# Optimization experiments

Hardware: AMD Instinct MI355X
Metric: run time of the kernel (lower is better)

Reference implementation:

```python
import jax, jax.numpy as jnp
import numpy as np

B, N, DIN, DOUT = 32, 1024, 256, 256


def setup_inputs() -> dict:
    key = jax.random.key(0)
    ks = jax.random.split(key, 7)
    s = 1.0 / np.sqrt(DIN)
    return {
        "x": jax.random.normal(ks[0], (B, N, DIN), dtype=jnp.float32),
        "Wq": jax.random.uniform(ks[1], (DOUT, DIN), minval=-s, maxval=s, dtype=jnp.float32),
        "bq": jax.random.uniform(ks[2], (DOUT,), minval=-s, maxval=s, dtype=jnp.float32),
        "Wk": jax.random.uniform(ks[3], (DOUT, DIN), minval=-s, maxval=s, dtype=jnp.float32),
        "bk": jax.random.uniform(ks[4], (DOUT,), minval=-s, maxval=s, dtype=jnp.float32),
        "Wv": jax.random.uniform(ks[5], (DOUT, DIN), minval=-s, maxval=s, dtype=jnp.float32),
        "bv": jax.random.uniform(ks[6], (DOUT,), minval=-s, maxval=s, dtype=jnp.float32),
    }


def reference(x, Wq, bq, Wk, bk, Wv, bv):
    # q, k, v: (B, N, Dout)
    q = jnp.einsum("bnd,od->bno", x, Wq) + bq
    k = jnp.einsum("bnd,od->bno", x, Wk) + bk
    v = jnp.einsum("bnd,od->bno", x, Wv) + bv
    # logits: (B, N, N) = q @ k^T per batch
    logits = jnp.einsum("bnd,bmd->bnm", q, k)
    # NOTE: softmax over the BATCH dim (axis=0), as in the original module
    attn = jax.nn.softmax(logits, axis=0)
    out = jnp.einsum("bnm,bmd->bnd", attn, v)  # (B, N, Dout)
    return out
```

## Files before the change

### kernel.cpp

```cpp
#include <hip/hip_runtime.h>

typedef __bf16 bf16x8 __attribute__((ext_vector_type(8)));
typedef __bf16 bf16x4 __attribute__((ext_vector_type(4)));
typedef float  f32x4  __attribute__((ext_vector_type(4)));

#define BM 128
#define BN 128
#define BK 64
#define LSD 144

__device__ __forceinline__ void g2l16(const void* g, void* l) {
    __builtin_amdgcn_global_load_lds((const __attribute__((address_space(1))) void*)g,
                                     (__attribute__((address_space(3))) void*)l, 16, 0, 0);
}

template<int EPI, int SWZ>
__global__ __launch_bounds__(256)
void gemm_nt(const __bf16* __restrict__ A, const __bf16* __restrict__ B,
             void* __restrict__ Cv, const float* __restrict__ bias,
             int lda, int ldb, int ldc, int K,
             long sA, long sB, long sC)
{
    __shared__ __align__(16) __bf16 smem[128 * LSD];
    __bf16* As = smem;
    __bf16* Bs = smem + BM * BK;

    const int tid  = threadIdx.x;
    const int w    = tid >> 6;
    const int lane = tid & 63;
    const int quad = lane >> 4;
    const int l16  = lane & 15;
    const int wm   = w & 1;
    const int wn   = w >> 1;

    int m0, n0, z;
    if constexpr (SWZ == 1) {
        const int id = blockIdx.x;
        const int x  = id & 7, s = id >> 3;
        z = x + ((s >> 6) << 3);
        const int t = s & 63;
        m0 = (t & 7) * BM;
        n0 = (t >> 3) * BN;
    } else {
        m0 = blockIdx.x * BM;
        n0 = blockIdx.y * BN;
        z  = blockIdx.z;
    }

    const __bf16* Ab = A + (size_t)z * sA;
    const __bf16* Bb = B + (size_t)z * sB;

    const int srow = (w << 3) + (lane >> 3);
    const int scol = ((lane & 7) ^ (lane >> 3)) << 3;
    char* ldsA = (char*)As + (size_t)w * 1024;
    char* ldsB = (char*)Bs + (size_t)w * 1024;

    const __bf16* Ag = Ab + (size_t)(m0 + srow) * lda + scol;
    const __bf16* Bg = Bb + (size_t)(n0 + srow) * ldb + scol;

    f32x4 acc[4][4] = {};

    for (int k0 = 0; k0 < K; k0 += BK) {
        __syncthreads();
        #pragma unroll
        for (int c = 0; c < 4; c++)
            g2l16(Ag + (size_t)(c * 32) * lda + k0, ldsA + c * 4096);
        #pragma unroll
        for (int c = 0; c < 4; c++)
            g2l16(Bg + (size_t)(c * 32) * ldb + k0, ldsB + c * 4096);
        __syncthreads();

        #pragma unroll
        for (int kk = 0; kk < BK; kk += 32) {
            const int ub = kk >> 3;
            bf16x8 a[4], b[4];
            #pragma unroll
            for (int mt = 0; mt < 4; mt++) {
                const int row = wm * 64 + mt * 16 + l16;
                const int cp  = ((quad + ub) ^ (row & 7)) << 3;
                a[mt] = *(const bf16x8*)&As[row * BK + cp];
            }
            #pragma unroll
            for (int nt = 0; nt < 4; nt++) {
                const int row = wn * 64 + nt * 16 + l16;
                const int cp  = ((quad + ub) ^ (row & 7)) << 3;
                b[nt] = *(const bf16x8*)&Bs[row * BK + cp];
            }
            #pragma unroll
            for (int mt = 0; mt < 4; mt++)
                #pragma unroll
                for (int nt = 0; nt < 4; nt++)
                    acc[mt][nt] = __builtin_amdgcn_mfma_f32_16x16x32_bf16(
                        a[mt], b[nt], acc[mt][nt], 0, 0, 0);
        }
    }

    __syncthreads();

    if constexpr (EPI == 2) {
        #pragma unroll
        for (int mt = 0; mt < 4; mt++) {
            const int rl = wm * 64 + mt * 16 + quad * 4;
            #pragma unroll
            for (int nt = 0; nt < 4; nt++) {
                const int cl = wn * 64 + nt * 16 + l16;
                #pragma unroll
                for (int r = 0; r < 4; r++)
                    smem[(rl + r) * LSD + cl] = (__bf16)__expf(acc[mt][nt][r]);
            }
        }
        __syncthreads();
        __bf16* C = (__bf16*)Cv + (size_t)z * sC;
        #pragma unroll
        for (int i = 0; i < 8; i++) {
            const int c   = tid + i * 256;
            const int row = c >> 4, c8 = (c & 15) << 3;
            *(bf16x8*)&C[(size_t)(m0 + row) * ldc + n0 + c8] =
                *(const bf16x8*)&smem[row * LSD + c8];
        }
    } else {
        if (z < 2) {
            #pragma unroll
            for (int mt = 0; mt < 4; mt++) {
                const int rl = wm * 64 + mt * 16 + quad * 4;
                #pragma unroll
                for (int nt = 0; nt < 4; nt++) {
                    const int cl = wn * 64 + nt * 16 + l16;
                    const float bn = bias[z * 256 + n0 + cl];
                    #pragma unroll
                    for (int r = 0; r < 4; r++)
                        smem[(rl + r) * LSD + cl] = (__bf16)(acc[mt][nt][r] + bn);
                }
            }
            __syncthreads();
            __bf16* C = (__bf16*)Cv + (size_t)z * sC;
            #pragma unroll
            for (int i = 0; i < 8; i++) {
                const int c   = tid + i * 256;
                const int row = c >> 4, c8 = (c & 15) << 3;
                *(bf16x8*)&C[(size_t)(m0 + row) * ldc + n0 + c8] =
                    *(const bf16x8*)&smem[row * LSD + c8];
            }
        } else {
            #pragma unroll
            for (int mt = 0; mt < 4; mt++) {
                const int ml = wm * 64 + mt * 16 + quad * 4;
                #pragma unroll
                for (int nt = 0; nt < 4; nt++) {
                    const int dl = wn * 64 + nt * 16 + l16;
                    const float bn = bias[z * 256 + n0 + dl];
                    bf16x4 pk;
                    #pragma unroll
                    for (int r = 0; r < 4; r++) pk[r] = (__bf16)(acc[mt][nt][r] + bn);
                    *(bf16x4*)&smem[dl * LSD + ml] = pk;
                }
            }
            __syncthreads();
            __bf16* C = (__bf16*)Cv + 2 * sC;
            const int bidx = m0 >> 10, mbase = m0 & 1023;
            #pragma unroll
            for (int i = 0; i < 8; i++) {
                const int c  = tid + i * 256;
                const int dl = c >> 4, m8 = (c & 15) << 3;
                *(bf16x8*)&C[(size_t)bidx * 262144 + (size_t)(n0 + dl) * 1024 + mbase + m8] =
                    *(const bf16x8*)&smem[dl * LSD + m8];
            }
        }
    }
}

__global__ __launch_bounds__(256)
void gemm_pv(const __bf16* __restrict__ E, const __bf16* __restrict__ vT,
             float* __restrict__ out)
{
    __shared__ __align__(16) __bf16 As[128 * 64];
    __shared__ __align__(16) __bf16 Bs[64 * 64];

    const int tid  = threadIdx.x;
    const int w    = tid >> 6;
    const int lane = tid & 63;
    const int quad = lane >> 4;
    const int l16  = lane & 15;
    const int wm   = w & 1;
    const int wn   = w >> 1;

    const int id = blockIdx.x;
    const int x  = id & 7, s = id >> 3;
    const int z  = x + ((s >> 5) << 3);
    const int t  = s & 31;
    const int m0 = (t & 7) * 128;
    const int n0 = (t >> 3) * 64;

    const __bf16* Eb = E  + (size_t)z * 1048576;
    const __bf16* Vb = vT + (size_t)z * 262144;
    float*        Ob = out + (size_t)z * 262144;

    const int srow = (w << 3) + (lane >> 3);
    const int scol = ((lane & 7) ^ (lane >> 3)) << 3;
    char* ldsA = (char*)As + (size_t)w * 1024;
    char* ldsB = (char*)Bs + (size_t)w * 1024;

    const __bf16* Ag = Eb + (size_t)(m0 + srow) * 1024 + scol;
    const __bf16* Bg = Vb + (size_t)(n0 + srow) * 1024 + scol;

    f32x4 acc[4][2] = {};

    for (int k0 = 0; k0 < 1024; k0 += BK) {
        __syncthreads();
        #pragma unroll
        for (int c = 0; c < 4; c++)
            g2l16(Ag + (size_t)(c * 32) * 1024 + k0, ldsA + c * 4096);
        #pragma unroll
        for (int c = 0; c < 2; c++)
            g2l16(Bg + (size_t)(c * 32) * 1024 + k0, ldsB + c * 4096);
        __syncthreads();

        #pragma unroll
        for (int kk = 0; kk < BK; kk += 32) {
            const int ub = kk >> 3;
            bf16x8 a[4], b[2];
            #pragma unroll
            for (int mt = 0; mt < 4; mt++) {
                const int row = wm * 64 + mt * 16 + l16;
                const int cp  = ((quad + ub) ^ (row & 7)) << 3;
                a[mt] = *(const bf16x8*)&As[row * BK + cp];
            }
            #pragma unroll
            for (int nt = 0; nt < 2; nt++) {
                const int row = wn * 32 + nt * 16 + l16;
                const int cp  = ((quad + ub) ^ (row & 7)) << 3;
                b[nt] = *(const bf16x8*)&Bs[row * BK + cp];
            }
            #pragma unroll
            for (int mt = 0; mt < 4; mt++)
                #pragma unroll
                for (int nt = 0; nt < 2; nt++)
                    acc[mt][nt] = __builtin_amdgcn_mfma_f32_16x16x32_bf16(
                        a[mt], b[nt], acc[mt][nt], 0, 0, 0);
        }
    }

    #pragma unroll
    for (int mt = 0; mt < 4; mt++) {
        const int mb = m0 + wm * 64 + mt * 16 + quad * 4;
        #pragma unroll
        for (int nt = 0; nt < 2; nt++) {
            const int n = n0 + wn * 32 + nt * 16 + l16;
            #pragma unroll
            for (int r = 0; r < 4; r++)
                Ob[(size_t)(mb + r) * 256 + n] = acc[mt][nt][r];
        }
    }
}

__global__ __launch_bounds__(256)
void cvt_all(const float* __restrict__ x,
             const float* __restrict__ Wq, const float* __restrict__ Wk,
             const float* __restrict__ Wv,
             const float* __restrict__ bq, const float* __restrict__ bk,
             const float* __restrict__ bv,
             __bf16* __restrict__ xb, __bf16* __restrict__ Wqb,
             float* __restrict__ bpack)
{
    const int i = blockIdx.x * 256 + threadIdx.x;
    if (i < 1073152) {
        const float* s; __bf16* d; int off;
        if (i < 1048576)      { s = x;  d = xb;            off = i; }
        else if (i < 1056768) { s = Wq; d = Wqb;           off = i - 1048576; }
        else if (i < 1064960) { s = Wk; d = Wqb + 131072;  off = i - 1056768; }
        else                  { s = Wv; d = Wqb + 262144;  off = i - 1064960; }
        const float4* s4 = (const float4*)s;
        const float4 f0 = s4[off * 2], f1 = s4[off * 2 + 1];
        bf16x8 o;
        o[0] = (__bf16)f0.x; o[1] = (__bf16)f0.y; o[2] = (__bf16)f0.z; o[3] = (__bf16)f0.w;
        o[4] = (__bf16)f1.x; o[5] = (__bf16)f1.y; o[6] = (__bf16)f1.z; o[7] = (__bf16)f1.w;
        ((bf16x8*)d)[off] = o;
    } else if (i < 1073344) {
        const int j = i - 1073152;
        const int sel = j >> 6, jj = j & 63;
        const float* s = sel == 0 ? bq : (sel == 1 ? bk : bv);
        ((float4*)bpack)[j] = ((const float4*)s)[jj];
    }
}

__global__ __launch_bounds__(256)
void softmax_norm(__bf16* __restrict__ E)
{
    const size_t p = (size_t)blockIdx.x * 256 + threadIdx.x;
    bf16x8* E8 = (bf16x8*)E;
    bf16x8 e[32];
    #pragma unroll
    for (int b = 0; b < 32; b++) e[b] = E8[(size_t)b * 131072 + p];
    float s[8] = {0.f, 0.f, 0.f, 0.f, 0.f, 0.f, 0.f, 0.f};
    #pragma unroll
    for (int b = 0; b < 32; b++)
        #pragma unroll
        for (int j = 0; j < 8; j++) s[j] += (float)e[b][j];
    float rs[8];
    #pragma unroll
    for (int j = 0; j < 8; j++) rs[j] = __builtin_amdgcn_rcpf(s[j]);
    #pragma unroll
    for (int b = 0; b < 32; b++) {
        bf16x8 o = e[b];
        #pragma unroll
        for (int j = 0; j < 8; j++) o[j] = (__bf16)((float)o[j] * rs[j]);
        E8[(size_t)b * 131072 + p] = o;
    }
}

extern "C" void kernel_launch(void* const* d_in, const int* in_sizes, int n_in,
                              void* d_out, int out_size, void* d_ws, size_t ws_size,
                              hipStream_t stream)
{
    const float* x  = (const float*)d_in[0];
    const float* Wq = (const float*)d_in[1];
    const float* bq = (const float*)d_in[2];
    const float* Wk = (const float*)d_in[3];
    const float* bk = (const float*)d_in[4];
    const float* Wv = (const float*)d_in[5];
    const float* bv = (const float*)d_in[6];
    float* out = (float*)d_out;

    char* ws = (char*)d_ws;
    __bf16* xb    = (__bf16*)(ws);
    __bf16* qkv   = (__bf16*)(ws + (16u << 20));
    __bf16* E     = (__bf16*)(ws + (64u << 20));
    __bf16* Wqb   = (__bf16*)(ws + (128u << 20));
    float*  bpack = (float*) (ws + (128u << 20) + (3u << 18));

    cvt_all<<<4194, 256, 0, stream>>>(x, Wq, Wk, Wv, bq, bk, bv, xb, Wqb, bpack);

    gemm_nt<4, 0><<<dim3(256, 2, 3), 256, 0, stream>>>(xb, Wqb, qkv, bpack,
                                                       256, 256, 256, 256,
                                                       0, 131072, 8388608);

    gemm_nt<2, 1><<<2048, 256, 0, stream>>>(qkv, qkv + 8388608, E, nullptr,
                                            256, 256, 1024, 256,
                                            262144, 262144, 1048576);

    softmax_norm<<<512, 256, 0, stream>>>(E);

    gemm_pv<<<1024, 256, 0, stream>>>(E, qkv + 2 * 8388608, out);
}
```

Measured before the change: 197.8 us.

## Fuse fp32-to-bf16 conversion into projection and softmax normalization into PV GEMM

Removes the separate conversion kernel by loading fp32 x and weights directly in the projection GEMM and converting to bf16 before the LDS store. The softmax pass now only computes per-position reciprocal sums into a bf16 buffer, and the PV GEMM scales E by those reciprocals while staging tiles, so E is never rewritten. PV tiles grow to 128x128, halving the grid. The trade is that the fused loads become register-staged instead of direct global-to-LDS, and PV now reads an extra 1024x1024 reciprocal matrix per tile.

```diff
diff --git a/kernel.cpp b/kernel.cpp
--- a/kernel.cpp
+++ b/kernel.cpp
@@ -4,9 +4,7 @@
 typedef __bf16 bf16x4 __attribute__((ext_vector_type(4)));
 typedef float  f32x4  __attribute__((ext_vector_type(4)));
 
-#define BM 128
-#define BN 128
-#define BK 64
+#define BK  64
 #define LSD 144
 
 __device__ __forceinline__ void g2l16(const void* g, void* l) {
@@ -14,16 +12,18 @@
                                      (__attribute__((address_space(3))) void*)l, 16, 0, 0);
 }
 
-template<int EPI, int SWZ>
+
 __global__ __launch_bounds__(256)
-void gemm_nt(const __bf16* __restrict__ A, const __bf16* __restrict__ B,
-             void* __restrict__ Cv, const float* __restrict__ bias,
-             int lda, int ldb, int ldc, int K,
-             long sA, long sB, long sC)
+void gemm_proj(const float* __restrict__ x,
+               const float* __restrict__ Wq, const float* __restrict__ Wk,
+               const float* __restrict__ Wv,
+               const float* __restrict__ bq, const float* __restrict__ bk,
+               const float* __restrict__ bv,
+               __bf16* __restrict__ qkv)
 {
     __shared__ __align__(16) __bf16 smem[128 * LSD];
     __bf16* As = smem;
-    __bf16* Bs = smem + BM * BK;
+    __bf16* Bs = smem + 128 * BK;
 
     const int tid  = threadIdx.x;
     const int w    = tid >> 6;
@@ -33,41 +33,43 @@
     const int wm   = w & 1;
     const int wn   = w >> 1;
 
-    int m0, n0, z;
-    if constexpr (SWZ == 1) {
-        const int id = blockIdx.x;
-        const int x  = id & 7, s = id >> 3;
-        z = x + ((s >> 6) << 3);
-        const int t = s & 63;
-        m0 = (t & 7) * BM;
-        n0 = (t >> 3) * BN;
-    } else {
-        m0 = blockIdx.x * BM;
-        n0 = blockIdx.y * BN;
-        z  = blockIdx.z;
-    }
-
-    const __bf16* Ab = A + (size_t)z * sA;
-    const __bf16* Bb = B + (size_t)z * sB;
+    const int m0 = blockIdx.x * 128;
+    const int n0 = blockIdx.y * 128;
+    const int z  = blockIdx.z;
+
+    const float* W    = z == 0 ? Wq : (z == 1 ? Wk : Wv);
+    const float* bias = z == 0 ? bq : (z == 1 ? bk : bv);
 
     const int srow = (w << 3) + (lane >> 3);
     const int scol = ((lane & 7) ^ (lane >> 3)) << 3;
-    char* ldsA = (char*)As + (size_t)w * 1024;
-    char* ldsB = (char*)Bs + (size_t)w * 1024;
-
-    const __bf16* Ag = Ab + (size_t)(m0 + srow) * lda + scol;
-    const __bf16* Bg = Bb + (size_t)(n0 + srow) * ldb + scol;
+    char* ldsA = (char*)As + w * 1024 + lane * 16;
+    char* ldsB = (char*)Bs + w * 1024 + lane * 16;
+
+    const float* Ag = x + (size_t)(m0 + srow) * 256 + scol;
+    const float* Bg = W + (size_t)(n0 + srow) * 256 + scol;
 
     f32x4 acc[4][4] = {};
 
-    for (int k0 = 0; k0 < K; k0 += BK) {
-        __syncthreads();
-        #pragma unroll
-        for (int c = 0; c < 4; c++)
-            g2l16(Ag + (size_t)(c * 32) * lda + k0, ldsA + c * 4096);
-        #pragma unroll
-        for (int c = 0; c < 4; c++)
-            g2l16(Bg + (size_t)(c * 32) * ldb + k0, ldsB + c * 4096);
+    for (int k0 = 0; k0 < 256; k0 += BK) {
+        __syncthreads();
+        #pragma unroll
+        for (int c = 0; c < 4; c++) {
+            const float* s = Ag + (size_t)(c * 32) * 256 + k0;
+            const float4 f0 = *(const float4*)s, f1 = *(const float4*)(s + 4);
+            bf16x8 o;
+            o[0] = (__bf16)f0.x; o[1] = (__bf16)f0.y; o[2] = (__bf16)f0.z; o[3] = (__bf16)f0.w;
+            o[4] = (__bf16)f1.x; o[5] = (__bf16)f1.y; o[6] = (__bf16)f1.z; o[7] = (__bf16)f1.w;
+            *(bf16x8*)(ldsA + c * 4096) = o;
+        }
+        #pragma unroll
+        for (int c = 0; c < 4; c++) {
+            const float* s = Bg + (size_t)(c * 32) * 256 + k0;
+            const float4 f0 = *(const float4*)s, f1 = *(const float4*)(s + 4);
+            bf16x8 o;
+            o[0] = (__bf16)f0.x; o[1] = (__bf16)f0.y; o[2] = (__bf16)f0.z; o[3] = (__bf16)f0.w;
+            o[4] = (__bf16)f1.x; o[5] = (__bf16)f1.y; o[6] = (__bf16)f1.z; o[7] = (__bf16)f1.w;
+            *(bf16x8*)(ldsB + c * 4096) = o;
+        }
         __syncthreads();
 
         #pragma unroll
@@ -96,85 +98,62 @@
     }
 
     __syncthreads();
-
-    if constexpr (EPI == 2) {
+    if (z < 2) {
         #pragma unroll
         for (int mt = 0; mt < 4; mt++) {
             const int rl = wm * 64 + mt * 16 + quad * 4;
             #pragma unroll
             for (int nt = 0; nt < 4; nt++) {
                 const int cl = wn * 64 + nt * 16 + l16;
+                const float bn = bias[n0 + cl];
                 #pragma unroll
                 for (int r = 0; r < 4; r++)
-                    smem[(rl + r) * LSD + cl] = (__bf16)__expf(acc[mt][nt][r]);
-            }
-        }
-        __syncthreads();
-        __bf16* C = (__bf16*)Cv + (size_t)z * sC;
+                    smem[(rl + r) * LSD + cl] = (__bf16)(acc[mt][nt][r] + bn);
+            }
+        }
+        __syncthreads();
+        __bf16* C = qkv + (size_t)z * 8388608;
         #pragma unroll
         for (int i = 0; i < 8; i++) {
             const int c   = tid + i * 256;
             const int row = c >> 4, c8 = (c & 15) << 3;
-            *(bf16x8*)&C[(size_t)(m0 + row) * ldc + n0 + c8] =
+            *(bf16x8*)&C[(size_t)(m0 + row) * 256 + n0 + c8] =
                 *(const bf16x8*)&smem[row * LSD + c8];
         }
     } else {
-        if (z < 2) {
-            #pragma unroll
-            for (int mt = 0; mt < 4; mt++) {
-                const int rl = wm * 64 + mt * 16 + quad * 4;
-                #pragma unroll
-                for (int nt = 0; nt < 4; nt++) {
-                    const int cl = wn * 64 + nt * 16 + l16;
-                    const float bn = bias[z * 256 + n0 + cl];
-                    #pragma unroll
-                    for (int r = 0; r < 4; r++)
-                        smem[(rl + r) * LSD + cl] = (__bf16)(acc[mt][nt][r] + bn);
-                }
-            }
-            __syncthreads();
-            __bf16* C = (__bf16*)Cv + (size_t)z * sC;
-            #pragma unroll
-            for (int i = 0; i < 8; i++) {
-                const int c   = tid + i * 256;
-                const int row = c >> 4, c8 = (c & 15) << 3;
-                *(bf16x8*)&C[(size_t)(m0 + row) * ldc + n0 + c8] =
-                    *(const bf16x8*)&smem[row * LSD + c8];
-            }
-        } else {
-            #pragma unroll
-            for (int mt = 0; mt < 4; mt++) {
-                const int ml = wm * 64 + mt * 16 + quad * 4;
-                #pragma unroll
-                for (int nt = 0; nt < 4; nt++) {
-                    const int dl = wn * 64 + nt * 16 + l16;
-                    const float bn = bias[z * 256 + n0 + dl];
-                    bf16x4 pk;
-                    #pragma unroll
-                    for (int r = 0; r < 4; r++) pk[r] = (__bf16)(acc[mt][nt][r] + bn);
-                    *(bf16x4*)&smem[dl * LSD + ml] = pk;
-                }
-            }
-            __syncthreads();
-            __bf16* C = (__bf16*)Cv + 2 * sC;
-            const int bidx = m0 >> 10, mbase = m0 & 1023;
-            #pragma unroll
-            for (int i = 0; i < 8; i++) {
-                const int c  = tid + i * 256;
-                const int dl = c >> 4, m8 = (c & 15) << 3;
-                *(bf16x8*)&C[(size_t)bidx * 262144 + (size_t)(n0 + dl) * 1024 + mbase + m8] =
-                    *(const bf16x8*)&smem[dl * LSD + m8];
-            }
+        #pragma unroll
+        for (int mt = 0; mt < 4; mt++) {
+            const int ml = wm * 64 + mt * 16 + quad * 4;
+            #pragma unroll
+            for (int nt = 0; nt < 4; nt++) {
+                const int dl = wn * 64 + nt * 16 + l16;
+                const float bn = bias[n0 + dl];
+                bf16x4 pk;
+                #pragma unroll
+                for (int r = 0; r < 4; r++) pk[r] = (__bf16)(acc[mt][nt][r] + bn);
+                *(bf16x4*)&smem[dl * LSD + ml] = pk;
+            }
+        }
+        __syncthreads();
+        __bf16* C = qkv + 2 * 8388608;
+        const int bidx = m0 >> 10, mbase = m0 & 1023;
+        #pragma unroll
+        for (int i = 0; i < 8; i++) {
+            const int c  = tid + i * 256;
+            const int dl = c >> 4, m8 = (c & 15) << 3;
+            *(bf16x8*)&C[(size_t)bidx * 262144 + (size_t)(n0 + dl) * 1024 + mbase + m8] =
+                *(const bf16x8*)&smem[dl * LSD + m8];
         }
     }
 }
 
 __global__ __launch_bounds__(256)
-void gemm_pv(const __bf16* __restrict__ E, const __bf16* __restrict__ vT,
-             float* __restrict__ out)
-{
-    __shared__ __align__(16) __bf16 As[128 * 64];
-    __shared__ __align__(16) __bf16 Bs[64 * 64];
+void gemm_logits(const __bf16* __restrict__ Q, const __bf16* __restrict__ Km,
+                 __bf16* __restrict__ E)
+{
+    __shared__ __align__(16) __bf16 smem[128 * LSD];
+    __bf16* As = smem;
+    __bf16* Bs = smem + 128 * BK;
 
     const int tid  = threadIdx.x;
     const int w    = tid >> 6;
@@ -186,39 +165,38 @@
 
     const int id = blockIdx.x;
     const int x  = id & 7, s = id >> 3;
-    const int z  = x + ((s >> 5) << 3);
-    const int t  = s & 31;
+    const int z  = x + ((s >> 6) << 3);
+    const int t  = s & 63;
     const int m0 = (t & 7) * 128;
-    const int n0 = (t >> 3) * 64;
-
-    const __bf16* Eb = E  + (size_t)z * 1048576;
-    const __bf16* Vb = vT + (size_t)z * 262144;
-    float*        Ob = out + (size_t)z * 262144;
+    const int n0 = (t >> 3) * 128;
+
+    const __bf16* Ab = Q  + (size_t)z * 262144;
+    const __bf16* Bb = Km + (size_t)z * 262144;
 
     const int srow = (w << 3) + (lane >> 3);
     const int scol = ((lane & 7) ^ (lane >> 3)) << 3;
     char* ldsA = (char*)As + (size_t)w * 1024;
     char* ldsB = (char*)Bs + (size_t)w * 1024;
 
-    const __bf16* Ag = Eb + (size_t)(m0 + srow) * 1024 + scol;
-    const __bf16* Bg = Vb + (size_t)(n0 + srow) * 1024 + scol;
-
-    f32x4 acc[4][2] = {};
-
-    for (int k0 = 0; k0 < 1024; k0 += BK) {
+    const __bf16* Ag = Ab + (size_t)(m0 + srow) * 256 + scol;
+    const __bf16* Bg = Bb + (size_t)(n0 + srow) * 256 + scol;
+
+    f32x4 acc[4][4] = {};
+
+    for (int k0 = 0; k0 < 256; k0 += BK) {
         __syncthreads();
         #pragma unroll
         for (int c = 0; c < 4; c++)
-            g2l16(Ag + (size_t)(c * 32) * 1024 + k0, ldsA + c * 4096);
-        #pragma unroll
-        for (int c = 0; c < 2; c++)
-            g2l16(Bg + (size_t)(c * 32) * 1024 + k0, ldsB + c * 4096);
+            g2l16(Ag + (size_t)(c * 32) * 256 + k0, ldsA + c * 4096);
+        #pragma unroll
+        for (int c = 0; c < 4; c++)
+            g2l16(Bg + (size_t)(c * 32) * 256 + k0, ldsB + c * 4096);
         __syncthreads();
 
         #pragma unroll
         for (int kk = 0; kk < BK; kk += 32) {
             const int ub = kk >> 3;
-            bf16x8 a[4], b[2];
+            bf16x8 a[4], b[4];
             #pragma unroll
             for (int mt = 0; mt < 4; mt++) {
                 const int row = wm * 64 + mt * 16 + l16;
@@ -226,85 +204,149 @@
                 a[mt] = *(const bf16x8*)&As[row * BK + cp];
             }
             #pragma unroll
-            for (int nt = 0; nt < 2; nt++) {
-                const int row = wn * 32 + nt * 16 + l16;
+            for (int nt = 0; nt < 4; nt++) {
+                const int row = wn * 64 + nt * 16 + l16;
                 const int cp  = ((quad + ub) ^ (row & 7)) << 3;
                 b[nt] = *(const bf16x8*)&Bs[row * BK + cp];
             }
             #pragma unroll
             for (int mt = 0; mt < 4; mt++)
                 #pragma unroll
-                for (int nt = 0; nt < 2; nt++)
+                for (int nt = 0; nt < 4; nt++)
                     acc[mt][nt] = __builtin_amdgcn_mfma_f32_16x16x32_bf16(
                         a[mt], b[nt], acc[mt][nt], 0, 0, 0);
         }
     }
 
+    __syncthreads();
+    #pragma unroll
+    for (int mt = 0; mt < 4; mt++) {
+        const int rl = wm * 64 + mt * 16 + quad * 4;
+        #pragma unroll
+        for (int nt = 0; nt < 4; nt++) {
+            const int cl = wn * 64 + nt * 16 + l16;
+            #pragma unroll
+            for (int r = 0; r < 4; r++)
+                smem[(rl + r) * LSD + cl] = (__bf16)__expf(acc[mt][nt][r]);
+        }
+    }
+    __syncthreads();
+    __bf16* C = E + (size_t)z * 1048576;
+    #pragma unroll
+    for (int i = 0; i < 8; i++) {
+        const int c   = tid + i * 256;
+        const int row = c >> 4, c8 = (c & 15) << 3;
+        *(bf16x8*)&C[(size_t)(m0 + row) * 1024 + n0 + c8] =
+            *(const bf16x8*)&smem[row * LSD + c8];
+    }
+}
+
+__global__ __launch_bounds__(256)
+void sum_rcp(const __bf16* __restrict__ E, __bf16* __restrict__ rcpS)
+{
+    const size_t p = (size_t)blockIdx.x * 256 + threadIdx.x;
+    const bf16x8* E8 = (const bf16x8*)E;
+    float s[8] = {0.f, 0.f, 0.f, 0.f, 0.f, 0.f, 0.f, 0.f};
+    #pragma unroll
+    for (int b = 0; b < 32; b++) {
+        const bf16x8 e = E8[(size_t)b * 131072 + p];
+        #pragma unroll
+        for (int j = 0; j < 8; j++) s[j] += (float)e[j];
+    }
+    bf16x8 o;
+    #pragma unroll
+    for (int j = 0; j < 8; j++) o[j] = (__bf16)__builtin_amdgcn_rcpf(s[j]);
+    ((bf16x8*)rcpS)[p] = o;
+}
+
+__global__ __launch_bounds__(256)
+void gemm_pv(const __bf16* __restrict__ E, const __bf16* __restrict__ rcpS,
+             const __bf16* __restrict__ vT, float* __restrict__ out)
+{
+    __shared__ __align__(16) __bf16 As[128 * BK];
+    __shared__ __align__(16) __bf16 Bs[128 * BK];
+
+    const int tid  = threadIdx.x;
+    const int w    = tid >> 6;
+    const int lane = tid & 63;
+    const int quad = lane >> 4;
+    const int l16  = lane & 15;
+    const int wm   = w & 1;
+    const int wn   = w >> 1;
+
+    const int id = blockIdx.x;
+    const int x  = id & 7, s = id >> 3;
+    const int z  = x + ((s >> 4) << 3);
+    const int t  = s & 15;
+    const int m0 = (t & 7) * 128;
+    const int n0 = (t >> 3) * 128;
+
+    const __bf16* Eb = E  + (size_t)z * 1048576;
+    const __bf16* Vb = vT + (size_t)z * 262144;
+    float*        Ob = out + (size_t)z * 262144;
+
+    const int srow = (w << 3) + (lane >> 3);
+    const int scol = ((lane & 7) ^ (lane >> 3)) << 3;
+    char* ldsAw = (char*)As + w * 1024 + lane * 16;
+    char* ldsB  = (char*)Bs + (size_t)w * 1024;
+
+    const __bf16* Ag = Eb   + (size_t)(m0 + srow) * 1024 + scol;
+    const __bf16* Rg = rcpS + (size_t)(m0 + srow) * 1024 + scol;
+    const __bf16* Bg = Vb   + (size_t)(n0 + srow) * 1024 + scol;
+
+    f32x4 acc[4][4] = {};
+
+    for (int k0 = 0; k0 < 1024; k0 += BK) {
+        __syncthreads();
+        #pragma unroll
+        for (int c = 0; c < 4; c++) {
+            const bf16x8 e  = *(const bf16x8*)(Ag + (size_t)(c * 32) * 1024 + k0);
+            const bf16x8 rs = *(const bf16x8*)(Rg + (size_t)(c * 32) * 1024 + k0);
+            bf16x8 o;
+            #pragma unroll
+            for (int j = 0; j < 8; j++) o[j] = (__bf16)((float)e[j] * (float)rs[j]);
+            *(bf16x8*)(ldsAw + c * 4096) = o;
+        }
+        #pragma unroll
+        for (int c = 0; c < 4; c++)
+            g2l16(Bg + (size_t)(c * 32) * 1024 + k0, ldsB + c * 4096);
+        __syncthreads();
+
+        #pragma unroll
+        for (int kk = 0; kk < BK; kk += 32) {
+            const int ub = kk >> 3;
+            bf16x8 a[4], b[4];
+            #pragma unroll
+            for (int mt = 0; mt < 4; mt++) {
+                const int row = wm * 64 + mt * 16 + l16;
+                const int cp  = ((quad + ub) ^ (row & 7)) << 3;
+                a[mt] = *(const bf16x8*)&As[row * BK + cp];
+            }
+            #pragma unroll
+            for (int nt = 0; nt < 4; nt++) {
+                const int row = wn * 64 + nt * 16 + l16;
+                const int cp  = ((quad + ub) ^ (row & 7)) << 3;
+                b[nt] = *(const bf16x8*)&Bs[row * BK + cp];
+            }
+            #pragma unroll
+            for (int mt = 0; mt < 4; mt++)
+                #pragma unroll
+                for (int nt = 0; nt < 4; nt++)
+                    acc[mt][nt] = __builtin_amdgcn_mfma_f32_16x16x32_bf16(
+                        a[mt], b[nt], acc[mt][nt], 0, 0, 0);
+        }
+    }
+
     #pragma unroll
     for (int mt = 0; mt < 4; mt++) {
         const int mb = m0 + wm * 64 + mt * 16 + quad * 4;
         #pragma unroll
-        for (int nt = 0; nt < 2; nt++) {
-            const int n = n0 + wn * 32 + nt * 16 + l16;
+        for (int nt = 0; nt < 4; nt++) {
+            const int n = n0 + wn * 64 + nt * 16 + l16;
             #pragma unroll
             for (int r = 0; r < 4; r++)
                 Ob[(size_t)(mb + r) * 256 + n] = acc[mt][nt][r];
         }
-    }
-}
-
-__global__ __launch_bounds__(256)
-void cvt_all(const float* __restrict__ x,
-             const float* __restrict__ Wq, const float* __restrict__ Wk,
-             const float* __restrict__ Wv,
-             const float* __restrict__ bq, const float* __restrict__ bk,
-             const float* __restrict__ bv,
-             __bf16* __restrict__ xb, __bf16* __restrict__ Wqb,
-             float* __restrict__ bpack)
-{
-    const int i = blockIdx.x * 256 + threadIdx.x;
-    if (i < 1073152) {
-        const float* s; __bf16* d; int off;
-        if (i < 1048576)      { s = x;  d = xb;            off = i; }
-        else if (i < 1056768) { s = Wq; d = Wqb;           off = i - 1048576; }
-        else if (i < 1064960) { s = Wk; d = Wqb + 131072;  off = i - 1056768; }
-        else                  { s = Wv; d = Wqb + 262144;  off = i - 1064960; }
-        const float4* s4 = (const float4*)s;
-        const float4 f0 = s4[off * 2], f1 = s4[off * 2 + 1];
-        bf16x8 o;
-        o[0] = (__bf16)f0.x; o[1] = (__bf16)f0.y; o[2] = (__bf16)f0.z; o[3] = (__bf16)f0.w;
-        o[4] = (__bf16)f1.x; o[5] = (__bf16)f1.y; o[6] = (__bf16)f1.z; o[7] = (__bf16)f1.w;
-        ((bf16x8*)d)[off] = o;
-    } else if (i < 1073344) {
-        const int j = i - 1073152;
-        const int sel = j >> 6, jj = j & 63;
-        const float* s = sel == 0 ? bq : (sel == 1 ? bk : bv);
-        ((float4*)bpack)[j] = ((const float4*)s)[jj];
-    }
-}
-
-__global__ __launch_bounds__(256)
-void softmax_norm(__bf16* __restrict__ E)
-{
-    const size_t p = (size_t)blockIdx.x * 256 + threadIdx.x;
-    bf16x8* E8 = (bf16x8*)E;
-    bf16x8 e[32];
-    #pragma unroll
-    for (int b = 0; b < 32; b++) e[b] = E8[(size_t)b * 131072 + p];
-    float s[8] = {0.f, 0.f, 0.f, 0.f, 0.f, 0.f, 0.f, 0.f};
-    #pragma unroll
-    for (int b = 0; b < 32; b++)
-        #pragma unroll
-        for (int j = 0; j < 8; j++) s[j] += (float)e[b][j];
-    float rs[8];
-    #pragma unroll
-    for (int j = 0; j < 8; j++) rs[j] = __builtin_amdgcn_rcpf(s[j]);
-    #pragma unroll
-    for (int b = 0; b < 32; b++) {
-        bf16x8 o = e[b];
-        #pragma unroll
-        for (int j = 0; j < 8; j++) o[j] = (__bf16)((float)o[j] * rs[j]);
-        E8[(size_t)b * 131072 + p] = o;
     }
 }
 
@@ -322,23 +364,15 @@
     float* out = (float*)d_out;
 
     char* ws = (char*)d_ws;
-    __bf16* xb    = (__bf16*)(ws);
-    __bf16* qkv   = (__bf16*)(ws + (16u << 20));
-    __bf16* E     = (__bf16*)(ws + (64u << 20));
-    __bf16* Wqb   = (__bf16*)(ws + (128u << 20));
-    float*  bpack = (float*) (ws + (128u << 20) + (3u << 18));
-
-    cvt_all<<<4194, 256, 0, stream>>>(x, Wq, Wk, Wv, bq, bk, bv, xb, Wqb, bpack);
-
-    gemm_nt<4, 0><<<dim3(256, 2, 3), 256, 0, stream>>>(xb, Wqb, qkv, bpack,
-                                                       256, 256, 256, 256,
-                                                       0, 131072, 8388608);
-
-    gemm_nt<2, 1><<<2048, 256, 0, stream>>>(qkv, qkv + 8388608, E, nullptr,
-                                            256, 256, 1024, 256,
-                                            262144, 262144, 1048576);
-
-    softmax_norm<<<512, 256, 0, stream>>>(E);
-
-    gemm_pv<<<1024, 256, 0, stream>>>(E, qkv + 2 * 8388608, out);
-}
+    __bf16* rcpS = (__bf16*)ws;
+    __bf16* qkv  = (__bf16*)(ws + (16u << 20));
+    __bf16* E    = (__bf16*)(ws + (64u << 20));
+
+    gemm_proj<<<dim3(256, 2, 3), 256, 0, stream>>>(x, Wq, Wk, Wv, bq, bk, bv, qkv);
+
+    gemm_logits<<<2048, 256, 0, stream>>>(qkv, qkv + 8388608, E);
+
+    sum_rcp<<<512, 256, 0, stream>>>(E, rcpS);
+
+    gemm_pv<<<512, 256, 0, stream>>>(E, rcpS, qkv + 2 * 8388608, out);
+}
```

Result: slower. 202.9 us (+2.6%).
